# Kernel tuning notes

Measured on AMD Instinct MI355X. Metric: run time of the kernel, lower is better.

The kernel has to match this reference:

```python
import math
import jax, jax.numpy as jnp
import numpy as np

L, H, W_SIZE, EPS = 4, 4, 64, 1e-5


def _sinusoidal_pe(T, D):
    pos = np.arange(T, dtype=np.float32)[:, None]
    div = np.exp(np.arange(0, D, 2, dtype=np.float32) * -(math.log(10000.0) / D))
    pe = np.zeros((T, D), dtype=np.float32)
    pe[:, 0::2] = np.sin(pos * div)
    pe[:, 1::2] = np.cos(pos * div)
    return jnp.asarray(pe)


def _layernorm(x, g, b):
    mu = jnp.mean(x, axis=-1, keepdims=True)
    var = jnp.mean(jnp.square(x - mu), axis=-1, keepdims=True)
    return (x - mu) * jax.lax.rsqrt(var + EPS) * g + b


def setup_inputs() -> dict:
    key = jax.random.key(0)
    B, T, D, F = 4, 2048, 256, 1024
    ks = jax.random.split(key, 8)
    s = 0.02
    return {
        "tokens": jax.random.normal(ks[0], (B, T, D), jnp.float32),
        "Wqkv": jax.random.normal(ks[1], (L, 3 * D, D), jnp.float32) * s,
        "bqkv": jnp.zeros((L, 3 * D), jnp.float32),
        "Wo": jax.random.normal(ks[2], (L, D, D), jnp.float32) * s,
        "bo": jnp.zeros((L, D), jnp.float32),
        "W1": jax.random.normal(ks[3], (L, F, D), jnp.float32) * s,
        "b1": jnp.zeros((L, F), jnp.float32),
        "W2": jax.random.normal(ks[4], (L, D, F), jnp.float32) * s,
        "b2": jnp.zeros((L, D), jnp.float32),
        "ln1_g": jnp.ones((L, D), jnp.float32),
        "ln1_b": jnp.zeros((L, D), jnp.float32),
        "ln2_g": jnp.ones((L, D), jnp.float32),
        "ln2_b": jnp.zeros((L, D), jnp.float32),
        "lnf_g": jnp.ones((D,), jnp.float32),
        "lnf_b": jnp.zeros((D,), jnp.float32),
    }


def reference(tokens, Wqkv, bqkv, Wo, bo, W1, b1, W2, b2,
              ln1_g, ln1_b, ln2_g, ln2_b, lnf_g, lnf_b):
    B, T, D = tokens.shape
    hd = D // H
    x = tokens + _sinusoidal_pe(T, D)[None]  # (B,T,D)

    # sliding-window causal mask: i attends to max(0, i-W+1)..i
    idx = jnp.arange(T)
    i, j = idx[:, None], idx[None, :]
    allowed = (j <= i) & (j >= i - W_SIZE + 1)
    bias = jnp.where(allowed, 0.0, -1e9).astype(jnp.float32)  # (T,T)

    def step(x, p):
        Wqkv, bqkv, Wo, bo, W1, b1, W2, b2, g1, be1, g2, be2 = p
        x2 = _layernorm(x, g1, be1)
        qkv = x2 @ Wqkv.T + bqkv                      # (B,T,3D)
        q, k, v = jnp.split(qkv, 3, axis=-1)
        q = q.reshape(B, T, H, hd)
        k = k.reshape(B, T, H, hd)
        v = v.reshape(B, T, H, hd)
        scores = jnp.einsum("bthd,bshd->bhts", q, k) / math.sqrt(hd)
        attn = jax.nn.softmax(scores + bias, axis=-1)
        o = jnp.einsum("bhts,bshd->bthd", attn, v).reshape(B, T, D)
        x = x + o @ Wo.T + bo
        x3 = _layernorm(x, g2, be2)
        h = jax.nn.gelu(x3 @ W1.T + b1, approximate=False)
        x = x + h @ W2.T + b2
        return x, None

    x, _ = jax.lax.scan(step, x, (Wqkv, bqkv, Wo, bo, W1, b1, W2, b2,
                                  ln1_g, ln1_b, ln2_g, ln2_b))
    return _layernorm(x, lnf_g, lnf_b)
```

## Files before the change

kernel.cpp:

```cpp
#include <hip/hip_runtime.h>
#include <hip/hip_bf16.h>
#include <math.h>

#define BB 4
#define TT 2048
#define DD 256
#define FF 1024
#define NL 4

typedef __bf16 bf16x8 __attribute__((ext_vector_type(8)));
typedef float f32x4 __attribute__((ext_vector_type(4)));
typedef __hip_bfloat16 bf16;

__device__ __forceinline__ void stage16(const bf16* gp, bf16* lp) {
  __builtin_amdgcn_global_load_lds(
      (const __attribute__((address_space(1))) unsigned int*)gp,
      (__attribute__((address_space(3))) unsigned int*)lp, 16, 0, 0);
}

__device__ __forceinline__ float gelu_f(float v) {
  float x = fabsf(v) * 0.70710678118654752f;
  float t = 1.0f / fmaf(0.3275911f, x, 1.0f);
  float p = t * fmaf(t, fmaf(t, fmaf(t, fmaf(t, 1.061405429f, -1.453152027f),
                                     1.421413741f), -0.284496736f), 0.254829592f);
  float erfv = copysignf(1.0f - p * __expf(-x * x), v);
  return 0.5f * v * (1.0f + erfv);
}

__global__ __launch_bounds__(256) void prologue_kernel(
    const float4* __restrict__ wq, const float4* __restrict__ wo,
    const float4* __restrict__ w1, const float4* __restrict__ w2,
    ushort4* __restrict__ dst,
    const float* __restrict__ tokens, const float* __restrict__ g,
    const float* __restrict__ b, float* __restrict__ x,
    bf16* __restrict__ sb) {
  if (blockIdx.x < 3072) {
    int gi = blockIdx.x * 256 + threadIdx.x;
    const float4* src;
    int off;
    if (gi < 196608)      { src = wq; off = gi; }
    else if (gi < 262144) { src = wo; off = gi - 196608; }
    else if (gi < 524288) { src = w1; off = gi - 262144; }
    else                  { src = w2; off = gi - 524288; }
    float4 v = src[off];
    ushort4 o;
    o.x = __hip_bfloat16_raw(__float2bfloat16(v.x)).x;
    o.y = __hip_bfloat16_raw(__float2bfloat16(v.y)).x;
    o.z = __hip_bfloat16_raw(__float2bfloat16(v.z)).x;
    o.w = __hip_bfloat16_raw(__float2bfloat16(v.w)).x;
    dst[gi] = o;
    return;
  }
  int row = (blockIdx.x - 3072) * 4 + (threadIdx.x >> 6);
  int lane = threadIdx.x & 63;
  int t = row & (TT - 1);
  const float* xr = tokens + (size_t)row * DD;
  float v[4];
  float s = 0.f;
#pragma unroll
  for (int i = 0; i < 4; ++i) {
    int d = lane + 64 * i;
    float freq = expf((float)(d & ~1) * -(9.210340371976184f / 256.f));
    float ang = (float)t * freq;
    float pe = (d & 1) ? cosf(ang) : sinf(ang);
    v[i] = xr[d] + pe;
    s += v[i];
  }
#pragma unroll
  for (int off = 32; off; off >>= 1) s += __shfl_xor(s, off, 64);
  float mu = s * (1.f / DD);
  float vs = 0.f;
#pragma unroll
  for (int i = 0; i < 4; ++i) { float dd = v[i] - mu; vs = fmaf(dd, dd, vs); }
#pragma unroll
  for (int off = 32; off; off >>= 1) vs += __shfl_xor(vs, off, 64);
  float rr = rsqrtf(vs * (1.f / DD) + 1e-5f);
#pragma unroll
  for (int i = 0; i < 4; ++i) {
    int d = lane + 64 * i;
    x[(size_t)row * DD + d] = v[i];
    sb[(size_t)row * DD + d] = __float2bfloat16((v[i] - mu) * rr * g[d] + b[d]);
  }
}

template <int MW, int NW, int BK, int KTOT, int ACT, int OUTF>
__global__ __launch_bounds__(256) void mgemm_kernel(
    const bf16* __restrict__ A, const bf16* __restrict__ B,
    const float* __restrict__ bias, void* __restrict__ Cout,
    int N, int nN, int nM) {
  constexpr int BM = 32 * MW, BN = 32 * NW, ROWS = BM + BN;
  constexpr int NCH = BK / 32;
  constexpr int CHB = ROWS * 32;
  constexpr int RG = ROWS / 16;
  constexpr int NST = NCH * RG;
  __shared__ __align__(16) bf16 sm[NCH * CHB];
  const int tid = threadIdx.x;
  const int wave = tid >> 6, lane = tid & 63;
  const int bid = blockIdx.x;
  const int xcd = bid & 7, kk = bid >> 3;
  const int mt = xcd * (nM >> 3) + kk / nN;
  const int nt = kk - (kk / nN) * nN;
  const int m0 = mt * BM, n0 = nt * BN;
  const int wm = (wave >> 1) * (16 * MW), wn = (wave & 1) * (16 * NW);
  const int quad = lane >> 4, lr = lane & 15;
  const int srow = lane >> 2, scol = (lane & 3) * 8;

  f32x4 acc[MW][NW] = {};

  for (int kt = 0; kt < KTOT; kt += BK) {
    __syncthreads();
#pragma unroll
    for (int i = 0; i < NST / 4; ++i) {
      int inst = i * 4 + wave;
      int c = inst / RG, grp = inst - c * RG;
      int r = grp * 16 + srow;
      const bf16* gp =
          (r < BM) ? (A + (size_t)(m0 + r) * KTOT + kt + c * 32 + scol)
                   : (B + (size_t)(n0 + (r - BM)) * KTOT + kt + c * 32 + scol);
      stage16(gp, sm + c * CHB + grp * 512);
    }
    __syncthreads();
#pragma unroll
    for (int c = 0; c < NCH; ++c) {
      bf16x8 af[MW], bfr[NW];
#pragma unroll
      for (int mi = 0; mi < MW; ++mi)
        af[mi] = *(const bf16x8*)(sm + c * CHB + (wm + mi * 16 + lr) * 32 + quad * 8);
#pragma unroll
      for (int ni = 0; ni < NW; ++ni)
        bfr[ni] = *(const bf16x8*)(sm + c * CHB + (BM + wn + ni * 16 + lr) * 32 + quad * 8);
#pragma unroll
      for (int mi = 0; mi < MW; ++mi)
#pragma unroll
        for (int ni = 0; ni < NW; ++ni)
          acc[mi][ni] = __builtin_amdgcn_mfma_f32_16x16x32_bf16(
              af[mi], bfr[ni], acc[mi][ni], 0, 0, 0);
    }
  }

#pragma unroll
  for (int mi = 0; mi < MW; ++mi)
#pragma unroll
    for (int ni = 0; ni < NW; ++ni) {
      int col = n0 + wn + ni * 16 + lr;
      float bv = bias[col];
#pragma unroll
      for (int r = 0; r < 4; ++r) {
        int row = m0 + wm + mi * 16 + quad * 4 + r;
        float v = acc[mi][ni][r] + bv;
        if (ACT == 1) v = gelu_f(v);
        if (OUTF) ((float*)Cout)[(size_t)row * N + col] = v;
        else ((bf16*)Cout)[(size_t)row * N + col] = __float2bfloat16(v);
      }
    }
}

template <int KTOT>
__global__ __launch_bounds__(256) void mgemm_ln_kernel(
    const bf16* __restrict__ A, const bf16* __restrict__ B,
    const float* __restrict__ bias, const float* __restrict__ res,
    const float* __restrict__ g, const float* __restrict__ bb,
    float* __restrict__ xout, bf16* __restrict__ yout) {
  constexpr int BM = 32, ROWS = BM + 256;
  constexpr int BK = 64, NCH = BK / 32;
  constexpr int CHB = ROWS * 32;
  constexpr int RG = ROWS / 16;
  constexpr int NST = NCH * RG;
  __shared__ __align__(16) bf16 sm[NCH * CHB];
  __shared__ float red1[4][BM], red2[4][BM];
  const int tid = threadIdx.x;
  const int wave = tid >> 6, lane = tid & 63;
  const int quad = lane >> 4, lr = lane & 15;
  const int m0 = blockIdx.x * BM;
  const int srow = lane >> 2, scol = (lane & 3) * 8;

  f32x4 acc[2][4] = {};

  for (int kt = 0; kt < KTOT; kt += BK) {
    __syncthreads();
#pragma unroll
    for (int i = 0; i < NST / 4; ++i) {
      int inst = i * 4 + wave;
      int c = inst / RG, grp = inst - c * RG;
      int r = grp * 16 + srow;
      const bf16* gp =
          (r < BM) ? (A + (size_t)(m0 + r) * KTOT + kt + c * 32 + scol)
                   : (B + (size_t)(r - BM) * KTOT + kt + c * 32 + scol);
      stage16(gp, sm + c * CHB + grp * 512);
    }
    __syncthreads();
#pragma unroll
    for (int c = 0; c < NCH; ++c) {
      bf16x8 af[2], bfr[4];
#pragma unroll
      for (int mi = 0; mi < 2; ++mi)
        af[mi] = *(const bf16x8*)(sm + c * CHB + (mi * 16 + lr) * 32 + quad * 8);
#pragma unroll
      for (int ni = 0; ni < 4; ++ni)
        bfr[ni] = *(const bf16x8*)(sm + c * CHB + (BM + wave * 64 + ni * 16 + lr) * 32 + quad * 8);
#pragma unroll
      for (int mi = 0; mi < 2; ++mi)
#pragma unroll
        for (int ni = 0; ni < 4; ++ni)
          acc[mi][ni] = __builtin_amdgcn_mfma_f32_16x16x32_bf16(
              af[mi], bfr[ni], acc[mi][ni], 0, 0, 0);
    }
  }

  float v[2][4][4];
  float s1[2][4] = {}, s2[2][4] = {};
#pragma unroll
  for (int mi = 0; mi < 2; ++mi)
#pragma unroll
    for (int ni = 0; ni < 4; ++ni) {
      int col = wave * 64 + ni * 16 + lr;
      float bv = bias[col];
#pragma unroll
      for (int r = 0; r < 4; ++r) {
        int row = m0 + mi * 16 + quad * 4 + r;
        float val = acc[mi][ni][r] + bv + res[(size_t)row * DD + col];
        v[mi][ni][r] = val;
        s1[mi][r] += val;
        s2[mi][r] = fmaf(val, val, s2[mi][r]);
      }
    }
#pragma unroll
  for (int mi = 0; mi < 2; ++mi)
#pragma unroll
    for (int r = 0; r < 4; ++r) {
#pragma unroll
      for (int off = 8; off; off >>= 1) {
        s1[mi][r] += __shfl_xor(s1[mi][r], off, 64);
        s2[mi][r] += __shfl_xor(s2[mi][r], off, 64);
      }
    }
  if (lr == 0) {
#pragma unroll
    for (int mi = 0; mi < 2; ++mi)
#pragma unroll
      for (int r = 0; r < 4; ++r) {
        red1[wave][mi * 16 + quad * 4 + r] = s1[mi][r];
        red2[wave][mi * 16 + quad * 4 + r] = s2[mi][r];
      }
  }
  __syncthreads();
#pragma unroll
  for (int mi = 0; mi < 2; ++mi)
#pragma unroll
    for (int r = 0; r < 4; ++r) {
      int rl = mi * 16 + quad * 4 + r;
      float ssum = red1[0][rl] + red1[1][rl] + red1[2][rl] + red1[3][rl];
      float qsum = red2[0][rl] + red2[1][rl] + red2[2][rl] + red2[3][rl];
      float mu = ssum * (1.f / DD);
      float var = qsum * (1.f / DD) - mu * mu;
      float rr = rsqrtf(var + 1e-5f);
      int row = m0 + rl;
#pragma unroll
      for (int ni = 0; ni < 4; ++ni) {
        int col = wave * 64 + ni * 16 + lr;
        float y = (v[mi][ni][r] - mu) * rr * g[col] + bb[col];
        yout[(size_t)row * DD + col] = __float2bfloat16(y);
        xout[(size_t)row * DD + col] = v[mi][ni][r];
      }
    }
}

template <int FIN>
__global__ __launch_bounds__(256) void rln_kernel(
    const bf16* __restrict__ go, const float* __restrict__ xin,
    const float* __restrict__ g, const float* __restrict__ b,
    float* __restrict__ xout, bf16* __restrict__ sbout,
    float* __restrict__ out) {
  int row = blockIdx.x * 4 + (threadIdx.x >> 6);
  int lane = threadIdx.x & 63;
  const bf16* gr = go + (size_t)row * DD;
  const float* xr = xin + (size_t)row * DD;
  float v[4];
  float s = 0.f;
#pragma unroll
  for (int i = 0; i < 4; ++i) {
    int d = lane + 64 * i;
    v[i] = __bfloat162float(gr[d]) + xr[d];
    s += v[i];
  }
#pragma unroll
  for (int off = 32; off; off >>= 1) s += __shfl_xor(s, off, 64);
  float mu = s * (1.f / DD);
  float vs = 0.f;
#pragma unroll
  for (int i = 0; i < 4; ++i) { float dd = v[i] - mu; vs = fmaf(dd, dd, vs); }
#pragma unroll
  for (int off = 32; off; off >>= 1) vs += __shfl_xor(vs, off, 64);
  float rr = rsqrtf(vs * (1.f / DD) + 1e-5f);
#pragma unroll
  for (int i = 0; i < 4; ++i) {
    int d = lane + 64 * i;
    float y = (v[i] - mu) * rr * g[d] + b[d];
    if (FIN) {
      out[(size_t)row * DD + d] = y;
    } else {
      xout[(size_t)row * DD + d] = v[i];
      sbout[(size_t)row * DD + d] = __float2bfloat16(y);
    }
  }
}

__global__ __launch_bounds__(256) void attn_kernel(const bf16* __restrict__ qkv,
                                                   bf16* __restrict__ o) {
  __shared__ __align__(16) bf16 KsPs[128 * 72];
  __shared__ __align__(16) bf16 Vt[64 * 136];
  const int bh = blockIdx.y;
  const int b = bh >> 2, h = bh & 3;
  const int t0 = blockIdx.x * 64;
  const int sbase = t0 - 63;
  const int tid = threadIdx.x;

  const bf16* kb = qkv + (size_t)(b * TT) * 768 + 256 + h * 64;
  const bf16* vb = kb + 256;
  union U8 { uint4 u; bf16 hx[8]; };
#pragma unroll
  for (int it = 0; it < 4; ++it) {
    int f = tid + it * 256;
    int si = f >> 3;
    int c8 = f & 7;
    int s = sbase + si;
    U8 kr, vr;
    kr.u = make_uint4(0, 0, 0, 0); vr.u = make_uint4(0, 0, 0, 0);
    if (s >= 0 && s < TT) {
      kr.u = *(const uint4*)&kb[(size_t)s * 768 + 8 * c8];
      vr.u = *(const uint4*)&vb[(size_t)s * 768 + 8 * c8];
    }
    *(uint4*)&KsPs[si * 72 + c8 * 8] = kr.u;
    int pc = (si >> 3) ^ c8;
#pragma unroll
    for (int j = 0; j < 8; ++j) Vt[(c8 * 8 + j) * 136 + pc * 8 + (si & 7)] = vr.hx[j];
  }
  __syncthreads();

  const int wave = tid >> 6, lane = tid & 63;
  const int quad = lane >> 4, lr = lane & 15;

  const bf16* qrow = qkv + (size_t)(b * TT + t0 + wave * 16 + lr) * 768 + h * 64;
  bf16x8 qa0 = *(const bf16x8*)(qrow + quad * 8);
  bf16x8 qa1 = *(const bf16x8*)(qrow + 32 + quad * 8);
  f32x4 sc[8];
#pragma unroll
  for (int c = 0; c < 8; ++c) {
    f32x4 a = {};
    bf16x8 kf0 = *(const bf16x8*)&KsPs[(c * 16 + lr) * 72 + quad * 8];
    a = __builtin_amdgcn_mfma_f32_16x16x32_bf16(qa0, kf0, a, 0, 0, 0);
    bf16x8 kf1 = *(const bf16x8*)&KsPs[(c * 16 + lr) * 72 + 32 + quad * 8];
    a = __builtin_amdgcn_mfma_f32_16x16x32_bf16(qa1, kf1, a, 0, 0, 0);
    sc[c] = a;
  }
  __syncthreads();

#pragma unroll
  for (int reg = 0; reg < 4; ++reg) {
    int dt = wave * 16 + quad * 4 + reg;
    float pv[8];
    float mx = -1e30f;
#pragma unroll
    for (int c = 0; c < 8; ++c) {
      int si = c * 16 + lr;
      float v = sc[c][reg] * 0.125f;
      bool ok = (si >= dt) && (si <= dt + 63) && (sbase + si >= 0);
      v = ok ? v : -1e30f;
      pv[c] = v;
      mx = fmaxf(mx, v);
    }
#pragma unroll
    for (int off = 8; off; off >>= 1) mx = fmaxf(mx, __shfl_xor(mx, off, 64));
    float l = 0.f;
#pragma unroll
    for (int c = 0; c < 8; ++c) { float e = __expf(pv[c] - mx); pv[c] = e; l += e; }
#pragma unroll
    for (int off = 8; off; off >>= 1) l += __shfl_xor(l, off, 64);
    float rinv = 1.f / l;
#pragma unroll
    for (int c = 0; c < 8; ++c)
      KsPs[(wave * 16 + quad * 4 + reg) * 136 + c * 16 + lr] = __float2bfloat16(pv[c] * rinv);
  }

  bf16* obase = o + (size_t)(b * TT) * DD + h * 64;
#pragma unroll
  for (int ct = 0; ct < 4; ++ct) {
    f32x4 acc = {};
#pragma unroll
    for (int kk = 0; kk < 4; ++kk) {
      bf16x8 pa = *(const bf16x8*)&KsPs[(wave * 16 + lr) * 136 + kk * 32 + quad * 8];
      int dd = ct * 16 + lr;
      bf16x8 vf = *(const bf16x8*)&Vt[dd * 136 + (((kk * 4 + quad) ^ (dd >> 3)) * 8)];
      acc = __builtin_amdgcn_mfma_f32_16x16x32_bf16(pa, vf, acc, 0, 0, 0);
    }
#pragma unroll
    for (int reg = 0; reg < 4; ++reg) {
      int t = t0 + wave * 16 + quad * 4 + reg;
      obase[(size_t)t * DD + ct * 16 + lr] = __float2bfloat16(acc[reg]);
    }
  }
}

extern "C" void kernel_launch(void* const* d_in, const int* in_sizes, int n_in,
                              void* d_out, int out_size, void* d_ws, size_t ws_size,
                              hipStream_t stream) {
  const float* tokens = (const float*)d_in[0];
  const float* Wqkv = (const float*)d_in[1];
  const float* bqkv = (const float*)d_in[2];
  const float* Wo   = (const float*)d_in[3];
  const float* bo   = (const float*)d_in[4];
  const float* W1   = (const float*)d_in[5];
  const float* b1   = (const float*)d_in[6];
  const float* W2   = (const float*)d_in[7];
  const float* b2   = (const float*)d_in[8];
  const float* ln1g = (const float*)d_in[9];
  const float* ln1b = (const float*)d_in[10];
  const float* ln2g = (const float*)d_in[11];
  const float* ln2b = (const float*)d_in[12];
  const float* lnfg = (const float*)d_in[13];
  const float* lnfb = (const float*)d_in[14];
  float* out = (float*)d_out;

  const int M = BB * TT;
  const int ND = M * DD;

  float* x = (float*)d_ws;
  bf16* sb  = (bf16*)(x + ND);
  bf16* big = sb + (size_t)M * DD;
  bf16* wqb = big + (size_t)M * FF;
  bf16* wob = wqb + (size_t)NL * 3 * DD * DD;
  bf16* w1b = wob + (size_t)NL * DD * DD;
  bf16* w2b = w1b + (size_t)NL * FF * DD;
  bf16* gbuf = w2b + (size_t)NL * DD * FF;

  prologue_kernel<<<3072 + M / 4, 256, 0, stream>>>(
      (const float4*)Wqkv, (const float4*)Wo, (const float4*)W1,
      (const float4*)W2, (ushort4*)wqb, tokens, ln1g, ln1b, x, sb);

  mgemm_kernel<2, 4, 128, 256, 0, 0><<<768, 256, 0, stream>>>(
      sb, wqb, bqkv, big, 768, 6, 128);

  for (int l = 0; l < NL; ++l) {
    attn_kernel<<<dim3(TT / 64, BB * 4), 256, 0, stream>>>(big, sb);
    mgemm_ln_kernel<256><<<M / 32, 256, 0, stream>>>(
        sb, wob + (size_t)l * DD * DD, bo + l * DD, x,
        ln2g + l * DD, ln2b + l * DD, x, sb);
    mgemm_kernel<2, 4, 128, 256, 1, 0><<<1024, 256, 0, stream>>>(
        sb, w1b + (size_t)l * FF * DD, b1 + l * FF, big, FF, 8, 128);
    mgemm_kernel<2, 2, 128, 1024, 0, 0><<<512, 256, 0, stream>>>(
        big, w2b + (size_t)l * DD * FF, b2 + l * DD, gbuf, DD, 4, 128);
    if (l < NL - 1) {
      rln_kernel<0><<<M / 4, 256, 0, stream>>>(
          gbuf, x, ln1g + (l + 1) * DD, ln1b + (l + 1) * DD, x, sb, nullptr);
      mgemm_kernel<2, 4, 128, 256, 0, 0><<<768, 256, 0, stream>>>(
          sb, wqb + (size_t)(l + 1) * 768 * DD, bqkv + (l + 1) * 768, big, 768, 6, 128);
    } else {
      rln_kernel<1><<<M / 4, 256, 0, stream>>>(
          gbuf, x, lnfg, lnfb, nullptr, nullptr, out);
    }
  }
}
```

Measured before the change: 354.5 us.

## Load GEMM operands directly from global into registers, dropping LDS staging

```diff
diff --git a/kernel.cpp b/kernel.cpp
--- a/kernel.cpp
+++ b/kernel.cpp
@@ -11,12 +11,6 @@
 typedef __bf16 bf16x8 __attribute__((ext_vector_type(8)));
 typedef float f32x4 __attribute__((ext_vector_type(4)));
 typedef __hip_bfloat16 bf16;
-
-__device__ __forceinline__ void stage16(const bf16* gp, bf16* lp) {
-  __builtin_amdgcn_global_load_lds(
-      (const __attribute__((address_space(1))) unsigned int*)gp,
-      (__attribute__((address_space(3))) unsigned int*)lp, 16, 0, 0);
-}
 
 __device__ __forceinline__ float gelu_f(float v) {
   float x = fabsf(v) * 0.70710678118654752f;
@@ -83,70 +77,52 @@
   }
 }
 
-template <int MW, int NW, int BK, int KTOT, int ACT, int OUTF>
-__global__ __launch_bounds__(256) void mgemm_kernel(
+template <int MW, int NW, int KTOT, int ACT, int OUTF>
+__global__ __launch_bounds__(256) void rgemm_kernel(
     const bf16* __restrict__ A, const bf16* __restrict__ B,
     const float* __restrict__ bias, void* __restrict__ Cout,
     int N, int nN, int nM) {
-  constexpr int BM = 32 * MW, BN = 32 * NW, ROWS = BM + BN;
-  constexpr int NCH = BK / 32;
-  constexpr int CHB = ROWS * 32;
-  constexpr int RG = ROWS / 16;
-  constexpr int NST = NCH * RG;
-  __shared__ __align__(16) bf16 sm[NCH * CHB];
   const int tid = threadIdx.x;
   const int wave = tid >> 6, lane = tid & 63;
   const int bid = blockIdx.x;
   const int xcd = bid & 7, kk = bid >> 3;
   const int mt = xcd * (nM >> 3) + kk / nN;
   const int nt = kk - (kk / nN) * nN;
-  const int m0 = mt * BM, n0 = nt * BN;
-  const int wm = (wave >> 1) * (16 * MW), wn = (wave & 1) * (16 * NW);
   const int quad = lane >> 4, lr = lane & 15;
-  const int srow = lane >> 2, scol = (lane & 3) * 8;
+  const int m0 = mt * (32 * MW) + (wave >> 1) * (16 * MW);
+  const int n0 = nt * (32 * NW) + (wave & 1) * (16 * NW);
+
+  const bf16* arow = A + (size_t)(m0 + lr) * KTOT + quad * 8;
+  const bf16* brow = B + (size_t)(n0 + lr) * KTOT + quad * 8;
 
   f32x4 acc[MW][NW] = {};
 
-  for (int kt = 0; kt < KTOT; kt += BK) {
-    __syncthreads();
-#pragma unroll
-    for (int i = 0; i < NST / 4; ++i) {
-      int inst = i * 4 + wave;
-      int c = inst / RG, grp = inst - c * RG;
-      int r = grp * 16 + srow;
-      const bf16* gp =
-          (r < BM) ? (A + (size_t)(m0 + r) * KTOT + kt + c * 32 + scol)
-                   : (B + (size_t)(n0 + (r - BM)) * KTOT + kt + c * 32 + scol);
-      stage16(gp, sm + c * CHB + grp * 512);
-    }
-    __syncthreads();
-#pragma unroll
-    for (int c = 0; c < NCH; ++c) {
-      bf16x8 af[MW], bfr[NW];
-#pragma unroll
-      for (int mi = 0; mi < MW; ++mi)
-        af[mi] = *(const bf16x8*)(sm + c * CHB + (wm + mi * 16 + lr) * 32 + quad * 8);
+#pragma unroll 4
+  for (int kt = 0; kt < KTOT; kt += 32) {
+    bf16x8 af[MW], bfr[NW];
+#pragma unroll
+    for (int mi = 0; mi < MW; ++mi)
+      af[mi] = *(const bf16x8*)(arow + (size_t)mi * 16 * KTOT + kt);
+#pragma unroll
+    for (int ni = 0; ni < NW; ++ni)
+      bfr[ni] = *(const bf16x8*)(brow + (size_t)ni * 16 * KTOT + kt);
+#pragma unroll
+    for (int mi = 0; mi < MW; ++mi)
 #pragma unroll
       for (int ni = 0; ni < NW; ++ni)
-        bfr[ni] = *(const bf16x8*)(sm + c * CHB + (BM + wn + ni * 16 + lr) * 32 + quad * 8);
-#pragma unroll
-      for (int mi = 0; mi < MW; ++mi)
-#pragma unroll
-        for (int ni = 0; ni < NW; ++ni)
-          acc[mi][ni] = __builtin_amdgcn_mfma_f32_16x16x32_bf16(
-              af[mi], bfr[ni], acc[mi][ni], 0, 0, 0);
-    }
+        acc[mi][ni] = __builtin_amdgcn_mfma_f32_16x16x32_bf16(
+            af[mi], bfr[ni], acc[mi][ni], 0, 0, 0);
   }
 
 #pragma unroll
   for (int mi = 0; mi < MW; ++mi)
 #pragma unroll
     for (int ni = 0; ni < NW; ++ni) {
-      int col = n0 + wn + ni * 16 + lr;
+      int col = n0 + ni * 16 + lr;
       float bv = bias[col];
 #pragma unroll
       for (int r = 0; r < 4; ++r) {
-        int row = m0 + wm + mi * 16 + quad * 4 + r;
+        int row = m0 + mi * 16 + quad * 4 + r;
         float v = acc[mi][ni][r] + bv;
         if (ACT == 1) v = gelu_f(v);
         if (OUTF) ((float*)Cout)[(size_t)row * N + col] = v;
@@ -155,114 +131,82 @@
     }
 }
 
-template <int KTOT>
-__global__ __launch_bounds__(256) void mgemm_ln_kernel(
+__global__ __launch_bounds__(256) void rgemm_ln_kernel(
     const bf16* __restrict__ A, const bf16* __restrict__ B,
     const float* __restrict__ bias, const float* __restrict__ res,
     const float* __restrict__ g, const float* __restrict__ bb,
     float* __restrict__ xout, bf16* __restrict__ yout) {
-  constexpr int BM = 32, ROWS = BM + 256;
-  constexpr int BK = 64, NCH = BK / 32;
-  constexpr int CHB = ROWS * 32;
-  constexpr int RG = ROWS / 16;
-  constexpr int NST = NCH * RG;
-  __shared__ __align__(16) bf16 sm[NCH * CHB];
-  __shared__ float red1[4][BM], red2[4][BM];
+  constexpr int KTOT = 256;
+  __shared__ float red1[4][16], red2[4][16];
   const int tid = threadIdx.x;
   const int wave = tid >> 6, lane = tid & 63;
   const int quad = lane >> 4, lr = lane & 15;
-  const int m0 = blockIdx.x * BM;
-  const int srow = lane >> 2, scol = (lane & 3) * 8;
-
-  f32x4 acc[2][4] = {};
-
-  for (int kt = 0; kt < KTOT; kt += BK) {
-    __syncthreads();
-#pragma unroll
-    for (int i = 0; i < NST / 4; ++i) {
-      int inst = i * 4 + wave;
-      int c = inst / RG, grp = inst - c * RG;
-      int r = grp * 16 + srow;
-      const bf16* gp =
-          (r < BM) ? (A + (size_t)(m0 + r) * KTOT + kt + c * 32 + scol)
-                   : (B + (size_t)(r - BM) * KTOT + kt + c * 32 + scol);
-      stage16(gp, sm + c * CHB + grp * 512);
-    }
-    __syncthreads();
-#pragma unroll
-    for (int c = 0; c < NCH; ++c) {
-      bf16x8 af[2], bfr[4];
-#pragma unroll
-      for (int mi = 0; mi < 2; ++mi)
-        af[mi] = *(const bf16x8*)(sm + c * CHB + (mi * 16 + lr) * 32 + quad * 8);
-#pragma unroll
-      for (int ni = 0; ni < 4; ++ni)
-        bfr[ni] = *(const bf16x8*)(sm + c * CHB + (BM + wave * 64 + ni * 16 + lr) * 32 + quad * 8);
-#pragma unroll
-      for (int mi = 0; mi < 2; ++mi)
-#pragma unroll
-        for (int ni = 0; ni < 4; ++ni)
-          acc[mi][ni] = __builtin_amdgcn_mfma_f32_16x16x32_bf16(
-              af[mi], bfr[ni], acc[mi][ni], 0, 0, 0);
-    }
-  }
-
-  float v[2][4][4];
-  float s1[2][4] = {}, s2[2][4] = {};
-#pragma unroll
-  for (int mi = 0; mi < 2; ++mi)
+  const int m0 = blockIdx.x * 16;
+
+  const bf16* arow = A + (size_t)(m0 + lr) * KTOT + quad * 8;
+  const bf16* brow = B + (size_t)(wave * 64 + lr) * KTOT + quad * 8;
+
+  f32x4 acc[4] = {};
+#pragma unroll 4
+  for (int kt = 0; kt < KTOT; kt += 32) {
+    bf16x8 af = *(const bf16x8*)(arow + kt);
+    bf16x8 bfr[4];
+#pragma unroll
+    for (int ni = 0; ni < 4; ++ni)
+      bfr[ni] = *(const bf16x8*)(brow + (size_t)ni * 16 * KTOT + kt);
+#pragma unroll
+    for (int ni = 0; ni < 4; ++ni)
+      acc[ni] = __builtin_amdgcn_mfma_f32_16x16x32_bf16(af, bfr[ni], acc[ni], 0, 0, 0);
+  }
+
+  float v[4][4];
+  float s1[4] = {}, s2[4] = {};
+#pragma unroll
+  for (int ni = 0; ni < 4; ++ni) {
+    int col = wave * 64 + ni * 16 + lr;
+    float bv = bias[col];
+#pragma unroll
+    for (int r = 0; r < 4; ++r) {
+      int row = m0 + quad * 4 + r;
+      float val = acc[ni][r] + bv + res[(size_t)row * DD + col];
+      v[ni][r] = val;
+      s1[r] += val;
+      s2[r] = fmaf(val, val, s2[r]);
+    }
+  }
+#pragma unroll
+  for (int r = 0; r < 4; ++r) {
+#pragma unroll
+    for (int off = 8; off; off >>= 1) {
+      s1[r] += __shfl_xor(s1[r], off, 64);
+      s2[r] += __shfl_xor(s2[r], off, 64);
+    }
+  }
+  if (lr == 0) {
+#pragma unroll
+    for (int r = 0; r < 4; ++r) {
+      red1[wave][quad * 4 + r] = s1[r];
+      red2[wave][quad * 4 + r] = s2[r];
+    }
+  }
+  __syncthreads();
+#pragma unroll
+  for (int r = 0; r < 4; ++r) {
+    int rl = quad * 4 + r;
+    float ssum = red1[0][rl] + red1[1][rl] + red1[2][rl] + red1[3][rl];
+    float qsum = red2[0][rl] + red2[1][rl] + red2[2][rl] + red2[3][rl];
+    float mu = ssum * (1.f / DD);
+    float var = qsum * (1.f / DD) - mu * mu;
+    float rr = rsqrtf(var + 1e-5f);
+    int row = m0 + rl;
 #pragma unroll
     for (int ni = 0; ni < 4; ++ni) {
       int col = wave * 64 + ni * 16 + lr;
-      float bv = bias[col];
-#pragma unroll
-      for (int r = 0; r < 4; ++r) {
-        int row = m0 + mi * 16 + quad * 4 + r;
-        float val = acc[mi][ni][r] + bv + res[(size_t)row * DD + col];
-        v[mi][ni][r] = val;
-        s1[mi][r] += val;
-        s2[mi][r] = fmaf(val, val, s2[mi][r]);
-      }
-    }
-#pragma unroll
-  for (int mi = 0; mi < 2; ++mi)
-#pragma unroll
-    for (int r = 0; r < 4; ++r) {
-#pragma unroll
-      for (int off = 8; off; off >>= 1) {
-        s1[mi][r] += __shfl_xor(s1[mi][r], off, 64);
-        s2[mi][r] += __shfl_xor(s2[mi][r], off, 64);
-      }
-    }
-  if (lr == 0) {
-#pragma unroll
-    for (int mi = 0; mi < 2; ++mi)
-#pragma unroll
-      for (int r = 0; r < 4; ++r) {
-        red1[wave][mi * 16 + quad * 4 + r] = s1[mi][r];
-        red2[wave][mi * 16 + quad * 4 + r] = s2[mi][r];
-      }
-  }
-  __syncthreads();
-#pragma unroll
-  for (int mi = 0; mi < 2; ++mi)
-#pragma unroll
-    for (int r = 0; r < 4; ++r) {
-      int rl = mi * 16 + quad * 4 + r;
-      float ssum = red1[0][rl] + red1[1][rl] + red1[2][rl] + red1[3][rl];
-      float qsum = red2[0][rl] + red2[1][rl] + red2[2][rl] + red2[3][rl];
-      float mu = ssum * (1.f / DD);
-      float var = qsum * (1.f / DD) - mu * mu;
-      float rr = rsqrtf(var + 1e-5f);
-      int row = m0 + rl;
-#pragma unroll
-      for (int ni = 0; ni < 4; ++ni) {
-        int col = wave * 64 + ni * 16 + lr;
-        float y = (v[mi][ni][r] - mu) * rr * g[col] + bb[col];
-        yout[(size_t)row * DD + col] = __float2bfloat16(y);
-        xout[(size_t)row * DD + col] = v[mi][ni][r];
-      }
-    }
+      float y = (v[ni][r] - mu) * rr * g[col] + bb[col];
+      yout[(size_t)row * DD + col] = __float2bfloat16(y);
+      xout[(size_t)row * DD + col] = v[ni][r];
+    }
+  }
 }
 
 template <int FIN>
@@ -437,22 +381,22 @@
       (const float4*)Wqkv, (const float4*)Wo, (const float4*)W1,
       (const float4*)W2, (ushort4*)wqb, tokens, ln1g, ln1b, x, sb);
 
-  mgemm_kernel<2, 4, 128, 256, 0, 0><<<768, 256, 0, stream>>>(
+  rgemm_kernel<2, 4, 256, 0, 0><<<768, 256, 0, stream>>>(
       sb, wqb, bqkv, big, 768, 6, 128);
 
   for (int l = 0; l < NL; ++l) {
     attn_kernel<<<dim3(TT / 64, BB * 4), 256, 0, stream>>>(big, sb);
-    mgemm_ln_kernel<256><<<M / 32, 256, 0, stream>>>(
+    rgemm_ln_kernel<<<M / 16, 256, 0, stream>>>(
         sb, wob + (size_t)l * DD * DD, bo + l * DD, x,
         ln2g + l * DD, ln2b + l * DD, x, sb);
-    mgemm_kernel<2, 4, 128, 256, 1, 0><<<1024, 256, 0, stream>>>(
+    rgemm_kernel<2, 4, 256, 1, 0><<<1024, 256, 0, stream>>>(
         sb, w1b + (size_t)l * FF * DD, b1 + l * FF, big, FF, 8, 128);
-    mgemm_kernel<2, 2, 128, 1024, 0, 0><<<512, 256, 0, stream>>>(
+    rgemm_kernel<2, 2, 1024, 0, 0><<<512, 256, 0, stream>>>(
         big, w2b + (size_t)l * DD * FF, b2 + l * DD, gbuf, DD, 4, 128);
     if (l < NL - 1) {
       rln_kernel<0><<<M / 4, 256, 0, stream>>>(
           gbuf, x, ln1g + (l + 1) * DD, ln1b + (l + 1) * DD, x, sb, nullptr);
-      mgemm_kernel<2, 4, 128, 256, 0, 0><<<768, 256, 0, stream>>>(
+      rgemm_kernel<2, 4, 256, 0, 0><<<768, 256, 0, stream>>>(
           sb, wqb + (size_t)(l + 1) * 768 * DD, bqkv + (l + 1) * 768, big, 768, 6, 128);
     } else {
       rln_kernel<1><<<M / 4, 256, 0, stream>>>(
```

Result: slower. 545.2 us (+53.8%).
